# Kernel optimization log

Hardware: AMD Instinct MI355X
Metric: run time of the kernel (lower is better)

The kernel has to match this reference:

```python
import jax, jax.numpy as jnp
import numpy as np

HID = 2048
H = 16
D_NOPE = 128
D_ROPE = 64
HEAD_DIM = D_NOPE + D_ROPE  # 192
V_DIM = 128
KV_RANK = 512
Q_RANK = 1536
THETA = 10000.0
EPS = 1e-6
B, S = 2, 2048


def _rope_cos_sin(seq_len):
    # half-dim frequencies: cos/sin have shape (seq_len, D_ROPE//2)
    inv_freq = 1.0 / (THETA ** (jnp.arange(0, D_ROPE, 2, dtype=jnp.float32) / D_ROPE))
    freqs = jnp.arange(seq_len, dtype=jnp.float32)[:, None] * inv_freq[None, :]
    return jnp.cos(freqs), jnp.sin(freqs)


def _apply_rope(x, cos, sin):
    # x: (..., D_ROPE); cos/sin broadcastable to (..., D_ROPE//2)
    half = x.shape[-1] // 2
    x1, x2 = x[..., :half], x[..., half:]
    return jnp.concatenate([x1 * cos - x2 * sin, x2 * cos + x1 * sin], axis=-1)


def _rmsnorm(x, w):
    ms = jnp.mean(jnp.square(x), axis=-1, keepdims=True)
    return x * jax.lax.rsqrt(ms + EPS) * w


def setup_inputs() -> dict:
    key = jax.random.key(0)
    ks = jax.random.split(key, 7)
    std = 0.02
    return {
        "x": jax.random.normal(ks[0], (B, S, HID), dtype=jnp.float32),
        "w_q_down": jax.random.normal(ks[1], (HID, Q_RANK), dtype=jnp.float32) * std,
        "w_q_up": jax.random.normal(ks[2], (Q_RANK, H * HEAD_DIM), dtype=jnp.float32) * std,
        "w_kv_down": jax.random.normal(ks[3], (HID, KV_RANK + D_ROPE), dtype=jnp.float32) * std,
        "kv_norm_w": jnp.ones((KV_RANK,), dtype=jnp.float32),
        "w_kv_up": jax.random.normal(ks[4], (KV_RANK, H * (D_NOPE + V_DIM)), dtype=jnp.float32) * std,
        "w_out": jax.random.normal(ks[5], (H * V_DIM, HID), dtype=jnp.float32) * std,
    }


def reference(x, w_q_down, w_q_up, w_kv_down, kv_norm_w, w_kv_up, w_out):
    b, s, _ = x.shape
    scale = 1.0 / np.sqrt(HEAD_DIM)

    # query: low-rank down then up, split into nope/rope parts
    q = (x @ w_q_down) @ w_q_up                      # (b, s, H*HEAD_DIM)
    q = q.reshape(b, s, H, HEAD_DIM)
    q_nope, q_rope = q[..., :D_NOPE], q[..., D_NOPE:]

    # KV: compressed latent + rope key component
    kv_full = x @ w_kv_down                          # (b, s, KV_RANK + D_ROPE)
    kv_c, k_rope = kv_full[..., :KV_RANK], kv_full[..., KV_RANK:]
    kv_c = _rmsnorm(kv_c, kv_norm_w)

    kv_exp = (kv_c @ w_kv_up).reshape(b, s, H, D_NOPE + V_DIM)
    k_nope, v = kv_exp[..., :D_NOPE], kv_exp[..., D_NOPE:]

    # RoPE (no past_kv -> q_offset = 0, kv_len = s)
    cos, sin = _rope_cos_sin(s)                      # (s, D_ROPE//2)
    cos4, sin4 = cos[None, :, None, :], sin[None, :, None, :]
    q_rope = _apply_rope(q_rope, cos4, sin4)         # (b, s, H, D_ROPE)
    k_rope = _apply_rope(k_rope, cos[None], sin[None])  # (b, s, D_ROPE)

    k_rope_h = jnp.broadcast_to(k_rope[:, :, None, :], (b, s, H, D_ROPE))
    k = jnp.concatenate([k_nope, k_rope_h], axis=-1)     # (b, s, H, HEAD_DIM)
    q_full = jnp.concatenate([q_nope, q_rope], axis=-1)  # (b, s, H, HEAD_DIM)

    # causal SDPA
    scores = jnp.einsum("bqhd,bkhd->bhqk", q_full, k) * scale
    causal = jnp.tril(jnp.ones((s, s), dtype=bool))
    scores = jnp.where(causal[None, None], scores, jnp.finfo(scores.dtype).min)
    attn = jax.nn.softmax(scores, axis=-1)
    out = jnp.einsum("bhqk,bkhd->bqhd", attn, v)     # (b, s, H, V_DIM)
    out = out.reshape(b, s, H * V_DIM)
    return out @ w_out
```

## Files before the change

kernel.cpp:

```cpp
#include <hip/hip_runtime.h>
#include <hip/hip_bf16.h>
#include <math.h>

#define HID    2048
#define NH     16
#define D_NOPE 128
#define D_ROPE 64
#define HD     192
#define V_DIM  128
#define KV_RANK 512
#define Q_RANK  1536
#define BATCH  2
#define SEQ    2048
#define ROWS   (BATCH*SEQ)

typedef __attribute__((ext_vector_type(8))) short short8;
typedef __attribute__((ext_vector_type(4))) float f32x4;

__device__ __forceinline__ unsigned short f2bf(float x) {
    unsigned int u = __float_as_uint(x);
    unsigned int r = (u + 0x7fffu + ((u >> 16) & 1u)) >> 16;
    return (unsigned short)r;
}
__device__ __forceinline__ float bf2f(unsigned short u) {
    return __uint_as_float((unsigned int)u << 16);
}

typedef const __attribute__((address_space(1))) unsigned int gu32;
typedef __attribute__((address_space(3))) unsigned int lu32;
__device__ __forceinline__ void gl_lds16(const void* g, void* l) {
    __builtin_amdgcn_global_load_lds((gu32*)g, (lu32*)l, 16, 0, 0);
}

template<int CTRL>
__device__ __forceinline__ float dpp_mv(float x) {
    return __int_as_float(__builtin_amdgcn_update_dpp(
        __float_as_int(x), __float_as_int(x), CTRL, 0xF, 0xF, true));
}
__device__ __forceinline__ float rowmax16(float x) {
    x = fmaxf(x, dpp_mv<0xB1>(x));
    x = fmaxf(x, dpp_mv<0x4E>(x));
    x = fmaxf(x, dpp_mv<0x141>(x));
    x = fmaxf(x, dpp_mv<0x140>(x));
    return x;
}

__global__ void rope_table_kernel(float* __restrict__ table) {
    int idx = blockIdx.x * 256 + threadIdx.x;
    int pos = idx >> 6, u = idx & 63;
    int i = u & 31;
    float invf = expf((float)i * (-9.210340371976184f / 32.0f));
    float ang = (float)pos * invf;
    table[idx] = (u < 32) ? cosf(ang) : sinf(ang);
}

__global__ __launch_bounds__(256) void convert_bf16_kernel(
    const float* __restrict__ src, unsigned short* __restrict__ dst)
{
    size_t i = (size_t)(blockIdx.x * 256 + threadIdx.x) * 4;
    float4 v = *(const float4*)(src + i);
    ushort4 u;
    u.x = f2bf(v.x); u.y = f2bf(v.y); u.z = f2bf(v.z); u.w = f2bf(v.w);
    *(ushort4*)(dst + i) = u;
}

__global__ __launch_bounds__(256) void transpose_bf16_kernel(
    const float* __restrict__ src, unsigned short* __restrict__ dst, int K, int N)
{
    __shared__ float T[64][65];
    const int n0 = blockIdx.x * 64, k0 = blockIdx.y * 64;
    const int t = threadIdx.x;
    const int c4 = t & 15, r = t >> 4;
    #pragma unroll
    for (int i = 0; i < 4; i++) {
        int row = r + i * 16;
        float4 v = *(const float4*)(src + (size_t)(k0 + row) * N + n0 + c4 * 4);
        T[row][c4*4+0] = v.x; T[row][c4*4+1] = v.y;
        T[row][c4*4+2] = v.z; T[row][c4*4+3] = v.w;
    }
    __syncthreads();
    #pragma unroll
    for (int i = 0; i < 4; i++) {
        int nrow = r + i * 16;
        ushort4 u;
        u.x = f2bf(T[c4*4+0][nrow]); u.y = f2bf(T[c4*4+1][nrow]);
        u.z = f2bf(T[c4*4+2][nrow]); u.w = f2bf(T[c4*4+3][nrow]);
        *(ushort4*)(dst + (size_t)(n0 + nrow) * K + k0 + c4 * 4) = u;
    }
}

template<int BN, bool OUT_BF16>
__global__ __launch_bounds__(256) void bgemm_kernel(
    const unsigned short* __restrict__ A,
    const unsigned short* __restrict__ Bt,
    void* __restrict__ Cv,
    int M, int N, int K)
{
    constexpr int NT = BN / 32;
    constexpr int NSLAB = 8 + BN / 16;
    const int tid  = threadIdx.x;
    const int w    = tid >> 6;
    const int lane = tid & 63;
    const int n16  = lane & 15, quad = lane >> 4;

    const int nb   = gridDim.x;
    const int T8   = nb >> 3;
    const int nbid = (blockIdx.x & 7) * T8 + (blockIdx.x >> 3);
    const int gx   = N / BN;
    const int m0 = (nbid / gx) * 128;
    const int n0 = (nbid % gx) * BN;
    const int moff = (w & 1) * 64;
    const int noff = (w >> 1) * (NT * 16);

    __shared__ unsigned short As[128 * 32];
    __shared__ unsigned short Bs[BN * 32];

    const unsigned short* gp[4];
    unsigned short* lp[4];
    int ns = 0;
    const int rl = lane >> 2, sc = lane & 3;
    for (int s = w; s < NSLAB; s += 4) {
        int kc = sc ^ (((s * 16 + rl) >> 1) & 3);
        if (s < 8) {
            gp[ns] = A + (size_t)(m0 + s * 16 + rl) * K + kc * 8;
            lp[ns] = As + s * 512;
        } else {
            int sb = s - 8;
            gp[ns] = Bt + (size_t)(n0 + sb * 16 + rl) * K + kc * 8;
            lp[ns] = Bs + sb * 512;
        }
        ns++;
    }

    const int swz = (quad ^ ((n16 >> 1) & 3)) * 8;
    int aoff[4], boff[NT];
    #pragma unroll
    for (int mt = 0; mt < 4; mt++) aoff[mt] = (moff + mt * 16 + n16) * 32 + swz;
    #pragma unroll
    for (int nt = 0; nt < NT; nt++) boff[nt] = (noff + nt * 16 + n16) * 32 + swz;

    f32x4 acc[4][NT];
    #pragma unroll
    for (int mt = 0; mt < 4; mt++)
        #pragma unroll
        for (int nt = 0; nt < NT; nt++) acc[mt][nt] = (f32x4){0.f, 0.f, 0.f, 0.f};

    for (int k0 = 0; k0 < K; k0 += 32) {
        #pragma unroll
        for (int j = 0; j < 4; j++) if (j < ns) gl_lds16(gp[j], lp[j]);
        #pragma unroll
        for (int j = 0; j < 4; j++) if (j < ns) gp[j] += 32;
        __syncthreads();

        short8 af[4], bfr[NT];
        #pragma unroll
        for (int mt = 0; mt < 4; mt++) af[mt] = *(const short8*)(As + aoff[mt]);
        #pragma unroll
        for (int nt = 0; nt < NT; nt++) bfr[nt] = *(const short8*)(Bs + boff[nt]);
        #pragma unroll
        for (int mt = 0; mt < 4; mt++)
            #pragma unroll
            for (int nt = 0; nt < NT; nt++)
                acc[mt][nt] = __builtin_amdgcn_mfma_f32_16x16x32_bf16(
                    af[mt], bfr[nt], acc[mt][nt], 0, 0, 0);
        __syncthreads();
    }

    #pragma unroll
    for (int mt = 0; mt < 4; mt++)
        #pragma unroll
        for (int nt = 0; nt < NT; nt++)
            #pragma unroll
            for (int r = 0; r < 4; r++) {
                size_t idx = (size_t)(m0 + moff + mt * 16 + quad * 4 + r) * N
                           + n0 + noff + nt * 16 + n16;
                if (OUT_BF16) ((unsigned short*)Cv)[idx] = f2bf(acc[mt][nt][r]);
                else          ((float*)Cv)[idx] = acc[mt][nt][r];
            }
}

__global__ __launch_bounds__(256) void kv_norm_rope_kernel(
    const float* __restrict__ kv_full,
    const float* __restrict__ w,
    const float* __restrict__ table,
    unsigned short* __restrict__ kv_cb,
    unsigned short* __restrict__ k_rope_b)
{
    const int row = blockIdx.x;
    const int tid = threadIdx.x;
    const float* src = kv_full + (size_t)row * 576;
    float v0 = src[tid], v1 = src[tid + 256];
    float ss = v0*v0 + v1*v1;
    #pragma unroll
    for (int off = 32; off > 0; off >>= 1) ss += __shfl_down(ss, off);
    __shared__ float red[4];
    __shared__ float msh;
    if ((tid & 63) == 0) red[tid >> 6] = ss;
    __syncthreads();
    if (tid == 0) msh = (red[0] + red[1] + red[2] + red[3]) * (1.0f / 512.0f);
    __syncthreads();
    float f = rsqrtf(msh + 1e-6f);
    kv_cb[(size_t)row * 512 + tid]       = f2bf(v0 * f * w[tid]);
    kv_cb[(size_t)row * 512 + tid + 256] = f2bf(v1 * f * w[tid + 256]);
    if (tid < 32) {
        int pos = row & (SEQ - 1);
        float c = table[pos*64 + tid], s = table[pos*64 + 32 + tid];
        float x1 = src[512 + tid], x2 = src[512 + 32 + tid];
        k_rope_b[(size_t)row * 64 + tid]      = f2bf(x1*c - x2*s);
        k_rope_b[(size_t)row * 64 + 32 + tid] = f2bf(x2*c + x1*s);
    }
}

__global__ __launch_bounds__(256) void q_rope_b_kernel(
    unsigned short* __restrict__ qb16, const float* __restrict__ table)
{
    int g = blockIdx.x * 8 + (threadIdx.x >> 5);
    int i = threadIdx.x & 31;
    int row = g >> 4, h = g & 15;
    size_t base = (size_t)row * (NH*HD) + h * HD + D_NOPE;
    int pos = row & (SEQ - 1);
    float c = table[pos*64 + i], s = table[pos*64 + 32 + i];
    float x1 = bf2f(qb16[base + i]), x2 = bf2f(qb16[base + 32 + i]);
    qb16[base + i]      = f2bf(x1*c - x2*s);
    qb16[base + 32 + i] = f2bf(x2*c + x1*s);
}

__global__ __launch_bounds__(256) void pack_vt_kernel(
    const unsigned short* __restrict__ kv_exp_b, unsigned short* __restrict__ Vmat)
{
    const int st = blockIdx.x;
    const int h  = blockIdx.y;
    const int b  = blockIdx.z;
    const int tid = threadIdx.x;
    const int s0 = st * 64;
    __shared__ float T[64][129];

    #pragma unroll
    for (int t = 0; t < 8; t++) {
        int idx = tid + t * 256;
        int tokr = idx >> 5, c4 = idx & 31;
        ushort4 u = *(const ushort4*)(kv_exp_b +
            ((size_t)(b*SEQ) + s0 + tokr) * 4096 + h*256 + 128 + c4*4);
        T[tokr][c4*4+0] = bf2f(u.x); T[tokr][c4*4+1] = bf2f(u.y);
        T[tokr][c4*4+2] = bf2f(u.z); T[tokr][c4*4+3] = bf2f(u.w);
    }
    __syncthreads();

    int d = tid >> 1, sh = (tid & 1) * 32;
    unsigned short* op = Vmat + ((size_t)((b*NH + h) * V_DIM + d)) * SEQ + s0 + sh;
    #pragma unroll
    for (int j = 0; j < 32; j += 2) {
        ushort2 u;
        u.x = f2bf(T[sh + j][d]);
        u.y = f2bf(T[sh + j + 1][d]);
        *(ushort2*)(op + j) = u;
    }
}

__global__ __launch_bounds__(256, 3) void flash_mfma_kernel(
    const unsigned short* __restrict__ qb16,
    const unsigned short* __restrict__ kv_exp_b,
    const unsigned short* __restrict__ k_rope_b,
    const unsigned short* __restrict__ Vmat,
    unsigned short* __restrict__ attnb)
{
    const int bid  = blockIdx.x;
    const int xcd  = bid & 7, slot = bid >> 3;
    const int grp  = xcd + 8 * (slot >> 5);
    const int qb   = 31 - (slot & 31);
    const int h    = grp & 15, b = grp >> 4;
    const int tid  = threadIdx.x;
    const int w    = tid >> 6;
    const int lane = tid & 63;
    const int n16  = lane & 15;
    const int quad = lane >> 4;

    const int q0 = qb * 64 + w * 16;
    const char* kNopeB = (const char*)(kv_exp_b + (size_t)b * SEQ * 4096 + h * 256);
    const char* kRopeB = (const char*)(k_rope_b + (size_t)b * SEQ * 64);
    const char* vByte  = (const char*)(Vmat + (size_t)(b*NH + h) * V_DIM * SEQ);

    __shared__ unsigned short Ks[2][6144];
    __shared__ unsigned short Vs[2][4096];
    __shared__ unsigned short Plds[4][16][40];

    const char* gK[2]; int lK[2];
    #pragma unroll
    for (int t = 0; t < 2; t++) {
        int idx = t * 256 + tid;
        int kc = idx >> 7, key = (idx >> 2) & 31, sc = idx & 3;
        int scs = sc ^ ((key >> 1) & 3);
        gK[t] = kNopeB + (size_t)key * 8192 + kc * 64 + scs * 16;
        lK[t] = idx * 16;
    }
    const char* gR; int lR;
    {
        int kc = tid >> 7, key = (tid >> 2) & 31, sc = tid & 3;
        int scs = sc ^ ((key >> 1) & 3);
        gR = kRopeB + (size_t)key * 128 + kc * 64 + scs * 16;
        lR = (512 + tid) * 16;
    }
    const char* gV[2]; int lV[2];
    #pragma unroll
    for (int t = 0; t < 2; t++) {
        int idx = t * 256 + tid;
        int d = idx >> 2, sc = idx & 3;
        int scs = sc ^ ((d >> 1) & 3);
        gV[t] = vByte + (size_t)d * (SEQ * 2) + scs * 16;
        lV[t] = idx * 16;
    }

    auto stage = [&](int kt, int bufsel) {
        const size_t koff = (size_t)kt * 32;
        #pragma unroll
        for (int t = 0; t < 2; t++)
            gl_lds16(gK[t] + koff * 8192, (char*)Ks[bufsel] + lK[t]);
        gl_lds16(gR + koff * 128, (char*)Ks[bufsel] + lR);
        #pragma unroll
        for (int t = 0; t < 2; t++)
            gl_lds16(gV[t] + koff * 2, (char*)Vs[bufsel] + lV[t]);
    };

    short8 qf[6];
    {
        const unsigned short* qp = qb16 + ((size_t)(b*SEQ) + q0 + n16) * (NH*HD)
                                 + h * HD + quad * 8;
        #pragma unroll
        for (int kc = 0; kc < 6; kc++)
            qf[kc] = *(const short8*)(qp + kc * 32);
    }

    short8 onesf;
    #pragma unroll
    for (int j = 0; j < 8; j++) onesf[j] = (short)0x3F80;

    f32x4 O[9];
    #pragma unroll
    for (int c = 0; c < 9; c++) O[c] = (f32x4){0.f, 0.f, 0.f, 0.f};
    float mrow[4] = {-INFINITY, -INFINITY, -INFINITY, -INFINITY};

    const float SCLOG2 = 0.10412779736150104f;
    const float THRRAW = 83.14f;
    const int swz = (quad ^ ((n16 >> 1) & 3)) * 8;
    const int ntB = 2 * qb + 2;

    stage(0, 0);
    int cur = 0;
    for (int kt = 0; kt < ntB; kt++) {
        __syncthreads();
        if (kt + 1 < ntB) stage(kt + 1, cur ^ 1);
        const int k0 = kt * 32;

        if (k0 <= q0 + 15) {
            const unsigned short* KsB = Ks[cur];
            const unsigned short* VsB = Vs[cur];

            f32x4 S[2];
            __builtin_amdgcn_s_setprio(1);
            #pragma unroll
            for (int half = 0; half < 2; half++) {
                f32x4 acc = (f32x4){0.f, 0.f, 0.f, 0.f};
                const int keyoff = (half * 16 + n16) * 32 + swz;
                #pragma unroll
                for (int kc = 0; kc < 6; kc++) {
                    short8 kf = *(const short8*)(KsB + kc * 1024 + keyoff);
                    acc = __builtin_amdgcn_mfma_f32_16x16x32_bf16(qf[kc], kf, acc, 0, 0, 0);
                }
                S[half] = acc;
            }
            __builtin_amdgcn_s_setprio(0);

            float p0[4], p1[4];
            if (k0 + 32 > q0) {
                #pragma unroll
                for (int r = 0; r < 4; r++) {
                    int row = q0 + quad*4 + r;
                    p0[r] = (k0 + n16      <= row) ? S[0][r] : -INFINITY;
                    p1[r] = (k0 + 16 + n16 <= row) ? S[1][r] : -INFINITY;
                }
            } else {
                #pragma unroll
                for (int r = 0; r < 4; r++) { p0[r] = S[0][r]; p1[r] = S[1][r]; }
            }

            float tmax[4];
            float growth = -INFINITY;
            #pragma unroll
            for (int r = 0; r < 4; r++) {
                tmax[r] = rowmax16(fmaxf(p0[r], p1[r]));
                growth = fmaxf(growth, tmax[r] - mrow[r]);
            }
            if (!__all(growth <= THRRAW)) {
                #pragma unroll
                for (int r = 0; r < 4; r++) {
                    float mnew = fmaxf(mrow[r], tmax[r]);
                    float alpha = exp2f((mrow[r] - mnew) * SCLOG2);
                    mrow[r] = mnew;
                    #pragma unroll
                    for (int c = 0; c < 9; c++) O[c][r] *= alpha;
                }
            }
            #pragma unroll
            for (int r = 0; r < 4; r++) {
                float e0 = exp2f((p0[r] - mrow[r]) * SCLOG2);
                float e1 = exp2f((p1[r] - mrow[r]) * SCLOG2);
                unsigned short* pw = &Plds[w][quad*4 + r][0];
                pw[n16]      = f2bf(e0);
                pw[16 + n16] = f2bf(e1);
            }

            short8 pf = *(const short8*)(&Plds[w][n16][quad * 8]);
            __builtin_amdgcn_s_setprio(1);
            #pragma unroll
            for (int c = 0; c < 8; c++) {
                short8 vf = *(const short8*)(VsB + (c * 16 + n16) * 32 + swz);
                O[c] = __builtin_amdgcn_mfma_f32_16x16x32_bf16(pf, vf, O[c], 0, 0, 0);
            }
            O[8] = __builtin_amdgcn_mfma_f32_16x16x32_bf16(pf, onesf, O[8], 0, 0, 0);
            __builtin_amdgcn_s_setprio(0);
        }
        cur ^= 1;
    }

    float invl[4];
    #pragma unroll
    for (int r = 0; r < 4; r++) invl[r] = 1.0f / O[8][r];
    #pragma unroll
    for (int c = 0; c < 8; c++) {
        #pragma unroll
        for (int r = 0; r < 4; r++) {
            size_t tok = (size_t)b * SEQ + q0 + quad*4 + r;
            attnb[tok * (NH*V_DIM) + h * V_DIM + c*16 + n16] = f2bf(O[c][r] * invl[r]);
        }
    }
}

extern "C" void kernel_launch(void* const* d_in, const int* in_sizes, int n_in,
                              void* d_out, int out_size, void* d_ws, size_t ws_size,
                              hipStream_t stream)
{
    const float* x         = (const float*)d_in[0];
    const float* w_q_down  = (const float*)d_in[1];
    const float* w_q_up    = (const float*)d_in[2];
    const float* w_kv_down = (const float*)d_in[3];
    const float* kv_norm_w = (const float*)d_in[4];
    const float* w_kv_up   = (const float*)d_in[5];
    const float* w_out     = (const float*)d_in[6];
    float* out = (float*)d_out;
    float* ws  = (float*)d_ws;

    float*          table    = ws;
    unsigned short* xb       = (unsigned short*)(ws + 131072);
    unsigned short* qdb      = (unsigned short*)(ws + 4325376);
    unsigned short* qb16     = (unsigned short*)(ws + 7471104);
    float*          kv_full  = ws + 13762560;
    unsigned short* kv_cb    = (unsigned short*)(ws + 16121856);
    unsigned short* k_rope_b = (unsigned short*)(ws + 17170432);
    unsigned short* kv_exp_b = (unsigned short*)(ws + 17301504);
    unsigned short* Vmat     = (unsigned short*)(ws + 25690112);
    unsigned short* attnb    = (unsigned short*)(ws + 29884416);
    unsigned short* wt1      = (unsigned short*)(ws + 34078720);
    unsigned short* wt2      = (unsigned short*)(ws + 35651584);
    unsigned short* wt3      = (unsigned short*)(ws + 38010880);
    unsigned short* wt4      = (unsigned short*)(ws + 38600704);
    unsigned short* wt5      = (unsigned short*)(ws + 39649280);

    rope_table_kernel<<<512, 256, 0, stream>>>(table);

    convert_bf16_kernel<<<ROWS*HID/1024, 256, 0, stream>>>(x, xb);
    transpose_bf16_kernel<<<dim3(1536/64, 2048/64), 256, 0, stream>>>(w_q_down, wt1, 2048, 1536);
    transpose_bf16_kernel<<<dim3(3072/64, 1536/64), 256, 0, stream>>>(w_q_up,   wt2, 1536, 3072);
    transpose_bf16_kernel<<<dim3(576/64,  2048/64), 256, 0, stream>>>(w_kv_down,wt3, 2048, 576);
    transpose_bf16_kernel<<<dim3(4096/64,  512/64), 256, 0, stream>>>(w_kv_up,  wt4, 512, 4096);
    transpose_bf16_kernel<<<dim3(2048/64, 2048/64), 256, 0, stream>>>(w_out,    wt5, 2048, 2048);

    bgemm_kernel<128, true><<<dim3(384),  256, 0, stream>>>(xb,  wt1, qdb,  ROWS, 1536, 2048);
    bgemm_kernel<128, true><<<dim3(768),  256, 0, stream>>>(qdb, wt2, qb16, ROWS, 3072, 1536);
    q_rope_b_kernel<<<8192, 256, 0, stream>>>(qb16, table);

    bgemm_kernel<64, false><<<dim3(288),  256, 0, stream>>>(xb, wt3, kv_full, ROWS, 576, 2048);
    kv_norm_rope_kernel<<<ROWS, 256, 0, stream>>>(kv_full, kv_norm_w, table, kv_cb, k_rope_b);
    bgemm_kernel<128, true><<<dim3(1024), 256, 0, stream>>>(kv_cb, wt4, kv_exp_b, ROWS, 4096, 512);
    pack_vt_kernel<<<dim3(SEQ/64, NH, BATCH), 256, 0, stream>>>(kv_exp_b, Vmat);

    flash_mfma_kernel<<<dim3(1024), 256, 0, stream>>>(qb16, kv_exp_b, k_rope_b, Vmat, attnb);

    bgemm_kernel<128, false><<<dim3(512), 256, 0, stream>>>(attnb, wt5, out, ROWS, 2048, 2048);
}
```

Measured before the change: 482.8 us.

## Fuse preprocessing launches, apply q RoPE inside flash kernel, use packed bf16 convert

Merges the rope table, x conversion and the five weight transposes into one block-indexed kernel, removing several launches. Drops the separate q RoPE pass, which read and wrote q in global memory, and applies the rotation to the Q fragments in registers when the flash kernel loads them. Replaces the manual float-to-bf16 rounding of softmax probabilities with the packed hardware convert instruction. This adds table loads and some VALU work to the attention prologue.

```diff
diff --git a/kernel.cpp b/kernel.cpp
--- a/kernel.cpp
+++ b/kernel.cpp
@@ -45,32 +45,49 @@
     return x;
 }
 
-__global__ void rope_table_kernel(float* __restrict__ table) {
-    int idx = blockIdx.x * 256 + threadIdx.x;
-    int pos = idx >> 6, u = idx & 63;
-    int i = u & 31;
-    float invf = expf((float)i * (-9.210340371976184f / 32.0f));
-    float ang = (float)pos * invf;
-    table[idx] = (u < 32) ? cosf(ang) : sinf(ang);
-}
-
-__global__ __launch_bounds__(256) void convert_bf16_kernel(
-    const float* __restrict__ src, unsigned short* __restrict__ dst)
+__global__ __launch_bounds__(256) void preprocess_kernel(
+    const float* __restrict__ x,
+    const float* __restrict__ w_q_down, const float* __restrict__ w_q_up,
+    const float* __restrict__ w_kv_down, const float* __restrict__ w_kv_up,
+    const float* __restrict__ w_out,
+    float* __restrict__ table, unsigned short* __restrict__ xb,
+    unsigned short* __restrict__ wt1, unsigned short* __restrict__ wt2,
+    unsigned short* __restrict__ wt3, unsigned short* __restrict__ wt4,
+    unsigned short* __restrict__ wt5)
 {
-    size_t i = (size_t)(blockIdx.x * 256 + threadIdx.x) * 4;
-    float4 v = *(const float4*)(src + i);
-    ushort4 u;
-    u.x = f2bf(v.x); u.y = f2bf(v.y); u.z = f2bf(v.z); u.w = f2bf(v.w);
-    *(ushort4*)(dst + i) = u;
-}
-
-__global__ __launch_bounds__(256) void transpose_bf16_kernel(
-    const float* __restrict__ src, unsigned short* __restrict__ dst, int K, int N)
-{
+    const int tid = threadIdx.x;
+    int bid = blockIdx.x;
+
+    if (bid < 512) {
+        int idx = bid * 256 + tid;
+        int pos = idx >> 6, u = idx & 63;
+        int i = u & 31;
+        float invf = expf((float)i * (-9.210340371976184f / 32.0f));
+        float ang = (float)pos * invf;
+        table[idx] = (u < 32) ? cosf(ang) : sinf(ang);
+        return;
+    }
+    bid -= 512;
+    if (bid < 8192) {
+        size_t i = (size_t)(bid * 256 + tid) * 4;
+        float4 v = *(const float4*)(x + i);
+        ushort4 u;
+        u.x = f2bf(v.x); u.y = f2bf(v.y); u.z = f2bf(v.z); u.w = f2bf(v.w);
+        *(ushort4*)(xb + i) = u;
+        return;
+    }
+    bid -= 8192;
+
+    const float* src; unsigned short* dst; int K, N, gx, lb;
+    if (bid < 768)       { src = w_q_down;  dst = wt1; K = 2048; N = 1536; gx = 24; lb = bid; }
+    else if (bid < 1920) { src = w_q_up;    dst = wt2; K = 1536; N = 3072; gx = 48; lb = bid - 768; }
+    else if (bid < 2208) { src = w_kv_down; dst = wt3; K = 2048; N = 576;  gx = 9;  lb = bid - 1920; }
+    else if (bid < 2720) { src = w_kv_up;   dst = wt4; K = 512;  N = 4096; gx = 64; lb = bid - 2208; }
+    else                 { src = w_out;     dst = wt5; K = 2048; N = 2048; gx = 32; lb = bid - 2720; }
+    const int n0 = (lb % gx) * 64, k0 = (lb / gx) * 64;
+
     __shared__ float T[64][65];
-    const int n0 = blockIdx.x * 64, k0 = blockIdx.y * 64;
-    const int t = threadIdx.x;
-    const int c4 = t & 15, r = t >> 4;
+    const int c4 = tid & 15, r = tid >> 4;
     #pragma unroll
     for (int i = 0; i < 4; i++) {
         int row = r + i * 16;
@@ -211,20 +228,6 @@
     }
 }
 
-__global__ __launch_bounds__(256) void q_rope_b_kernel(
-    unsigned short* __restrict__ qb16, const float* __restrict__ table)
-{
-    int g = blockIdx.x * 8 + (threadIdx.x >> 5);
-    int i = threadIdx.x & 31;
-    int row = g >> 4, h = g & 15;
-    size_t base = (size_t)row * (NH*HD) + h * HD + D_NOPE;
-    int pos = row & (SEQ - 1);
-    float c = table[pos*64 + i], s = table[pos*64 + 32 + i];
-    float x1 = bf2f(qb16[base + i]), x2 = bf2f(qb16[base + 32 + i]);
-    qb16[base + i]      = f2bf(x1*c - x2*s);
-    qb16[base + 32 + i] = f2bf(x2*c + x1*s);
-}
-
 __global__ __launch_bounds__(256) void pack_vt_kernel(
     const unsigned short* __restrict__ kv_exp_b, unsigned short* __restrict__ Vmat)
 {
@@ -262,6 +265,7 @@
     const unsigned short* __restrict__ kv_exp_b,
     const unsigned short* __restrict__ k_rope_b,
     const unsigned short* __restrict__ Vmat,
+    const float* __restrict__ table,
     unsigned short* __restrict__ attnb)
 {
     const int bid  = blockIdx.x;
@@ -328,6 +332,20 @@
         #pragma unroll
         for (int kc = 0; kc < 6; kc++)
             qf[kc] = *(const short8*)(qp + kc * 32);
+        const float* tb = table + (size_t)(q0 + n16) * 64 + quad * 8;
+        float4 c0 = *(const float4*)(tb);
+        float4 c1 = *(const float4*)(tb + 4);
+        float4 s0 = *(const float4*)(tb + 32);
+        float4 s1 = *(const float4*)(tb + 36);
+        float cs[8] = {c0.x,c0.y,c0.z,c0.w,c1.x,c1.y,c1.z,c1.w};
+        float sn[8] = {s0.x,s0.y,s0.z,s0.w,s1.x,s1.y,s1.z,s1.w};
+        #pragma unroll
+        for (int j = 0; j < 8; j++) {
+            float x1 = bf2f((unsigned short)qf[4][j]);
+            float x2 = bf2f((unsigned short)qf[5][j]);
+            qf[4][j] = (short)f2bf(x1*cs[j] - x2*sn[j]);
+            qf[5][j] = (short)f2bf(x2*cs[j] + x1*sn[j]);
+        }
     }
 
     short8 onesf;
@@ -404,9 +422,11 @@
             for (int r = 0; r < 4; r++) {
                 float e0 = exp2f((p0[r] - mrow[r]) * SCLOG2);
                 float e1 = exp2f((p1[r] - mrow[r]) * SCLOG2);
+                unsigned int pk;
+                asm("v_cvt_pk_bf16_f32 %0, %1, %2" : "=v"(pk) : "v"(e0), "v"(e1));
                 unsigned short* pw = &Plds[w][quad*4 + r][0];
-                pw[n16]      = f2bf(e0);
-                pw[16 + n16] = f2bf(e1);
+                pw[n16]      = (unsigned short)(pk & 0xffffu);
+                pw[16 + n16] = (unsigned short)(pk >> 16);
             }
 
             short8 pf = *(const short8*)(&Plds[w][n16][quad * 8]);
@@ -465,25 +485,19 @@
     unsigned short* wt4      = (unsigned short*)(ws + 38600704);
     unsigned short* wt5      = (unsigned short*)(ws + 39649280);
 
-    rope_table_kernel<<<512, 256, 0, stream>>>(table);
-
-    convert_bf16_kernel<<<ROWS*HID/1024, 256, 0, stream>>>(x, xb);
-    transpose_bf16_kernel<<<dim3(1536/64, 2048/64), 256, 0, stream>>>(w_q_down, wt1, 2048, 1536);
-    transpose_bf16_kernel<<<dim3(3072/64, 1536/64), 256, 0, stream>>>(w_q_up,   wt2, 1536, 3072);
-    transpose_bf16_kernel<<<dim3(576/64,  2048/64), 256, 0, stream>>>(w_kv_down,wt3, 2048, 576);
-    transpose_bf16_kernel<<<dim3(4096/64,  512/64), 256, 0, stream>>>(w_kv_up,  wt4, 512, 4096);
-    transpose_bf16_kernel<<<dim3(2048/64, 2048/64), 256, 0, stream>>>(w_out,    wt5, 2048, 2048);
+    preprocess_kernel<<<dim3(12448), 256, 0, stream>>>(
+        x, w_q_down, w_q_up, w_kv_down, w_kv_up, w_out,
+        table, xb, wt1, wt2, wt3, wt4, wt5);
 
     bgemm_kernel<128, true><<<dim3(384),  256, 0, stream>>>(xb,  wt1, qdb,  ROWS, 1536, 2048);
     bgemm_kernel<128, true><<<dim3(768),  256, 0, stream>>>(qdb, wt2, qb16, ROWS, 3072, 1536);
-    q_rope_b_kernel<<<8192, 256, 0, stream>>>(qb16, table);
 
     bgemm_kernel<64, false><<<dim3(288),  256, 0, stream>>>(xb, wt3, kv_full, ROWS, 576, 2048);
     kv_norm_rope_kernel<<<ROWS, 256, 0, stream>>>(kv_full, kv_norm_w, table, kv_cb, k_rope_b);
     bgemm_kernel<128, true><<<dim3(1024), 256, 0, stream>>>(kv_cb, wt4, kv_exp_b, ROWS, 4096, 512);
     pack_vt_kernel<<<dim3(SEQ/64, NH, BATCH), 256, 0, stream>>>(kv_exp_b, Vmat);
 
-    flash_mfma_kernel<<<dim3(1024), 256, 0, stream>>>(qb16, kv_exp_b, k_rope_b, Vmat, attnb);
+    flash_mfma_kernel<<<dim3(1024), 256, 0, stream>>>(qb16, kv_exp_b, k_rope_b, Vmat, table, attnb);
 
     bgemm_kernel<128, false><<<dim3(512), 256, 0, stream>>>(attnb, wt5, out, ROWS, 2048, 2048);
 }
```

Measured after the change: 461.3 us. 4.4% less time.
